# Performance work log

Measured on AMD Instinct MI355X. Metric: run time of the kernel, lower is better.

## Reference

```python
import jax, jax.numpy as jnp
import numpy as np

EMBED_DIM = 1024
NUM_HEADS = 16
HEAD_DIM = EMBED_DIM // NUM_HEADS


def setup_inputs() -> dict:
    key = jax.random.key(0)
    ks = jax.random.split(key, 7)
    B, S, E = 8, 1024, EMBED_DIM
    # xavier-uniform-like scale for in_proj_weight [3E, E]
    bound_in = float(np.sqrt(6.0 / (3 * E + E)))
    bound_out = float(np.sqrt(6.0 / (E + E)))
    return {
        "q": jax.random.normal(ks[0], (B, S, E), jnp.float32),
        "k": jax.random.normal(ks[1], (B, S, E), jnp.float32),
        "v": jax.random.normal(ks[2], (B, S, E), jnp.float32),
        "in_proj_weight": jax.random.uniform(ks[3], (3 * E, E), jnp.float32, -bound_in, bound_in),
        "in_proj_bias": jnp.zeros((3 * E,), jnp.float32),
        "out_proj_weight": jax.random.uniform(ks[4], (E, E), jnp.float32, -bound_out, bound_out),
        "out_proj_bias": jnp.zeros((E,), jnp.float32),
    }


def reference(q, k, v, in_proj_weight, in_proj_bias, out_proj_weight, out_proj_bias):
    B, S, E = q.shape
    H, D = NUM_HEADS, HEAD_DIM
    w_q, w_k, w_v = jnp.split(in_proj_weight, 3, axis=0)
    b_q, b_k, b_v = jnp.split(in_proj_bias, 3, axis=0)
    # packed in-projection: linear(x, W, b) = x @ W.T + b
    qp = q @ w_q.T + b_q
    kp = k @ w_k.T + b_k
    vp = v @ w_v.T + b_v
    # [B, S, E] -> [B, H, S, D]
    qh = qp.reshape(B, S, H, D).transpose(0, 2, 1, 3)
    kh = kp.reshape(B, S, H, D).transpose(0, 2, 1, 3)
    vh = vp.reshape(B, S, H, D).transpose(0, 2, 1, 3)
    scale = D ** -0.5
    # explicit full attention in fp32 (matches original fp32 cast path)
    scores = jnp.einsum("bhqd,bhkd->bhqk", qh, kh) * scale
    attn = jax.nn.softmax(scores, axis=-1)
    ctx = jnp.einsum("bhqk,bhkd->bhqd", attn, vh)  # [B, H, S, D]
    ctx = ctx.transpose(0, 2, 1, 3).reshape(B, S, E)
    out = ctx @ out_proj_weight.T + out_proj_bias
    return out
```

## Files before the change

### kernel.cpp

```cpp
#include <hip/hip_runtime.h>
#include <stdint.h>

#define TOK 8192
#define EDIM 1024
#define NH 16
#define HD 64
#define SEQ 1024
#define BATCH 8

typedef short bf16x8 __attribute__((ext_vector_type(8)));
typedef short bf16x4 __attribute__((ext_vector_type(4)));
typedef float f32x4 __attribute__((ext_vector_type(4)));
typedef float f32x16 __attribute__((ext_vector_type(16)));
typedef unsigned int u32x2 __attribute__((ext_vector_type(2)));
typedef unsigned int u32x4 __attribute__((ext_vector_type(4)));

__device__ __forceinline__ short f2bf(float f) {
  union { float f; uint32_t u; } c; c.f = f;
  uint32_t u = c.u;
  u += 0x7FFFu + ((u >> 16) & 1u);
  return (short)(u >> 16);
}
__device__ __forceinline__ float bf2f(short h) {
  union { uint32_t u; float f; } c; c.u = ((uint32_t)(uint16_t)h) << 16;
  return c.f;
}
__device__ __forceinline__ uint32_t bfr(float f) {
  union { float f; uint32_t u; } c; c.f = f;
  return (c.u + 0x8000u) >> 16;
}
__device__ __forceinline__ uint32_t cvtpk(float lo, float hi_) {
  uint32_t r;
  asm("v_cvt_pk_bf16_f32 %0, %1, %2" : "=v"(r) : "v"(lo), "v"(hi_));
  return r;
}

#define GLDS16(ldsp, gp) __builtin_amdgcn_global_load_lds( \
    (__attribute__((address_space(1))) void*)(gp),          \
    (__attribute__((address_space(3))) void*)(ldsp), 16, 0, 0)

__global__ __launch_bounds__(256) void cast_all(
    const float* __restrict__ q, const float* __restrict__ k,
    const float* __restrict__ v, const float* __restrict__ wi,
    const float* __restrict__ wo, short* __restrict__ dst) {
  const size_t NTOK = (size_t)TOK * EDIM;
  const size_t NWI = 3u * EDIM * EDIM;
  size_t i = ((size_t)blockIdx.x * 256 + threadIdx.x) * 4;
  const float* src;
  if (i < NTOK) src = q + i;
  else if (i < 2 * NTOK) src = k + (i - NTOK);
  else if (i < 3 * NTOK) src = v + (i - 2 * NTOK);
  else if (i < 3 * NTOK + NWI) src = wi + (i - 3 * NTOK);
  else src = wo + (i - 3 * NTOK - NWI);
  float4 f = *(const float4*)src;
  bf16x4 o;
  o[0] = f2bf(f.x); o[1] = f2bf(f.y); o[2] = f2bf(f.z); o[3] = f2bf(f.w);
  *(bf16x4*)(dst + i) = o;
}

#define GEMM_TILE9(KT, VMC, DOSTAGE)                                           \
  {                                                                            \
    asm volatile("s_waitcnt vmcnt(" VMC ")" ::: "memory");                     \
    __builtin_amdgcn_s_barrier();                                              \
    const short* Ab = lds + ((KT) & 3) * 12288;                                \
    const short* Bb = Ab + 8192;                                               \
    bf16x8 af[4], bv[4];                                                       \
    _Pragma("unroll")                                                          \
    for (int mi = 0; mi < 4; mi++)                                             \
      af[mi] = *(const bf16x8*)&Ab[(wrBase + mi * 16 + fr) * 32 + fg * 8];     \
    _Pragma("unroll")                                                          \
    for (int ni = 0; ni < 4; ni++)                                             \
      bv[ni] = *(const bf16x8*)&Bb[(wcBase + ni * 16 + fr) * 32 + fg * 8];     \
    if (DOSTAGE) {                                                             \
      char* d_ = (char*)lds + (((KT) + 3) & 3) * 24576 + t * 16;               \
      GLDS16(d_,         aS + ((KT) + 3) * 32);                                \
      GLDS16(d_ + 8192,  aS + ((KT) + 3) * 32 + 128 * 1024);                   \
      GLDS16(d_ + 16384, bS + ((KT) + 3) * 32);                                \
    }                                                                          \
    __builtin_amdgcn_s_setprio(1);                                             \
    _Pragma("unroll")                                                          \
    for (int mi = 0; mi < 4; mi++) {                                           \
      _Pragma("unroll")                                                        \
      for (int ni = 0; ni < 4; ni++)                                           \
        acc[mi][ni] = __builtin_amdgcn_mfma_f32_16x16x32_bf16(                 \
            af[mi], bv[ni], acc[mi][ni], 0, 0, 0);                             \
    }                                                                          \
    __builtin_amdgcn_s_setprio(0);                                             \
  }

template<int MODE>
__global__ __launch_bounds__(512, 1)
void gemm_bt9(const short* __restrict__ Abase, const short* __restrict__ Wbase,
              const float* __restrict__ biasBase, void* __restrict__ outv) {
  __shared__ short lds[49152];

  const int z = (MODE == 0) ? blockIdx.z : 0;
  const size_t NTOK = (size_t)TOK * EDIM;
  const short* A  = Abase + (size_t)z * NTOK;
  const short* Bw = Wbase + (size_t)z * EDIM * EDIM;
  const float* bias = biasBase + z * EDIM;

  const int t = threadIdx.x;
  const int l = t & 63, w = t >> 6;
  const int fr = l & 15, fg = l >> 4;
  const int wrBase = (w >> 1) * 64;
  const int wcBase = (w & 1) * 64;
  const int rowBase = blockIdx.x * 256;
  const int colBase = blockIdx.y * 128;

  f32x4 acc[4][4];
#pragma unroll
  for (int i = 0; i < 4; i++)
#pragma unroll
    for (int j = 0; j < 4; j++) acc[i][j] = (f32x4){0.f, 0.f, 0.f, 0.f};

  const short* aS = A  + (size_t)(rowBase + (t >> 2)) * EDIM + (t & 3) * 8;
  const short* bS = Bw + (size_t)(colBase + (t >> 2)) * EDIM + (t & 3) * 8;

#pragma unroll
  for (int s = 0; s < 3; s++) {
    char* d = (char*)lds + s * 24576 + t * 16;
    GLDS16(d,         aS + s * 32);
    GLDS16(d + 8192,  aS + s * 32 + 128 * 1024);
    GLDS16(d + 16384, bS + s * 32);
  }

#pragma unroll 1
  for (int kt = 0; kt < 30; kt++) {
    GEMM_TILE9(kt, "6", (kt <= 28));
  }
  GEMM_TILE9(30, "3", false);
  GEMM_TILE9(31, "0", false);

#pragma unroll
  for (int mi = 0; mi < 4; mi++)
#pragma unroll
    for (int ni = 0; ni < 4; ni++)
#pragma unroll
      for (int r = 0; r < 4; r++) {
        int grow = rowBase + wrBase + mi * 16 + fg * 4 + r;
        int gcol = colBase + wcBase + ni * 16 + fr;
        float v = acc[mi][ni][r] + bias[gcol];
        if (MODE == 0) {
          int b_ = grow >> 10, s_ = grow & 1023;
          int h_ = gcol >> 6,  d_ = gcol & 63;
          short* outp = (short*)outv + (size_t)z * NTOK;
          outp[((size_t)((b_ * NH + h_) * SEQ + s_) << 6) | d_] = f2bf(v);
        } else {
          ((float*)outv)[(size_t)grow * EDIM + gcol] = v;
        }
      }
}

__global__ __launch_bounds__(512)
void attn_fwd9(const short* __restrict__ proj, short* __restrict__ ctx) {
  __shared__ short lds[16384];

  const int t = threadIdx.x;
  const int l = t & 63, w = t >> 6;
  const int ln = l & 31, hi = l >> 5;

  const int n = blockIdx.x + 4 * (blockIdx.y + 16 * blockIdx.z);
  const int qt = (n >> 3) & 3;
  const int hl = (n & 7) | ((n >> 5) << 3);
  const int h = hl & 15, b = hl >> 4;

  const size_t NTOK = (size_t)TOK * EDIM;
  const size_t headOff = (size_t)(b * NH + h) * SEQ * HD;
  const short* Qp = proj + headOff;
  const short* Kp = proj + NTOK + headOff;
  const short* Vp = proj + 2 * NTOK + headOff;

  const int q0 = qt * 256;
  const int qrow = q0 + w * 32 + ln;

  const int kRow = t >> 3;
  const int kCol = ((t & 7) ^ (kRow & 7)) << 3;
  const int vd0  = w * 8;

  const float qscale = 0.18033688011112042f;
  bf16x8 bQ[4];
#pragma unroll
  for (int ds = 0; ds < 4; ds++) {
    bf16x8 v = *(const bf16x8*)(Qp + (size_t)qrow * HD + ds * 16 + hi * 8);
#pragma unroll
    for (int j = 0; j < 8; j++) v[j] = (short)bfr(bf2f(v[j]) * qscale);
    bQ[ds] = v;
  }

  float l_acc[4] = {0.f, 0.f, 0.f, 0.f};
  f32x16 ot[2];
#pragma unroll
  for (int i = 0; i < 16; i++) { ot[0][i] = 0.f; ot[1][i] = 0.f; }

  {
    GLDS16((char*)lds + t * 16, Kp + (size_t)kRow * HD + kCol);
    bf16x8 v0 = *(const bf16x8*)(Vp + (size_t)l * HD + vd0);
    char* VtB = (char*)lds + 8192;
#pragma unroll
    for (int jj = 0; jj < 8; jj++) {
      int d = vd0 + jj;
      *(short*)(VtB + d * 128 + (((l >> 3) ^ (d & 7)) << 4) + (l & 7) * 2) = v0[jj];
    }
  }
  __syncthreads();

  for (int jt = 0; jt < SEQ / 64; jt++) {
    const int bufByte = (jt & 1) << 14;
    const int nb = bufByte ^ (1 << 14);
    const bool have_next = (jt + 1 < SEQ / 64);

    bf16x8 nv0;
    if (have_next) {
      const int kv1 = (jt + 1) * 64;
      GLDS16((char*)lds + nb + t * 16, Kp + (size_t)(kv1 + kRow) * HD + kCol);
      nv0 = *(const bf16x8*)(Vp + (size_t)(kv1 + l) * HD + vd0);
    }

    f32x16 sa[2];
#pragma unroll
    for (int i = 0; i < 16; i++) { sa[0][i] = 0.f; sa[1][i] = 0.f; }
    __builtin_amdgcn_s_setprio(1);
#pragma unroll
    for (int ds = 0; ds < 4; ds++) {
#pragma unroll
      for (int kvb = 0; kvb < 2; kvb++) {
        int kv = kvb * 32 + ln;
        bf16x8 aK = *(const bf16x8*)((const char*)lds + bufByte + kv * 128 +
                                     (((ds * 2 + hi) ^ (kv & 7)) << 4));
        sa[kvb] = __builtin_amdgcn_mfma_f32_32x32x16_bf16(aK, bQ[ds], sa[kvb], 0, 0, 0);
      }
    }
    __builtin_amdgcn_s_setprio(0);

#pragma unroll
    for (int i = 0; i < 16; i++) {
      float p0 = exp2f(sa[0][i]);
      float p1 = exp2f(sa[1][i]);
      sa[0][i] = p0; sa[1][i] = p1;
      l_acc[i & 3] += p0 + p1;
    }

    bf16x8 pa[4];
#pragma unroll
    for (int ks = 0; ks < 4; ks++) {
      const int kvb = ks >> 1, hf = (ks & 1) * 8;
      uint32_t A1 = cvtpk(sa[kvb][hf + 0], sa[kvb][hf + 1]);
      uint32_t A2 = cvtpk(sa[kvb][hf + 2], sa[kvb][hf + 3]);
      uint32_t B1 = cvtpk(sa[kvb][hf + 4], sa[kvb][hf + 5]);
      uint32_t B2 = cvtpk(sa[kvb][hf + 6], sa[kvb][hf + 7]);
      u32x4 wds;
#if __has_builtin(__builtin_amdgcn_permlane32_swap)
      u32x2 r13 = __builtin_amdgcn_permlane32_swap(A1, B1, false, false);
      u32x2 r24 = __builtin_amdgcn_permlane32_swap(A2, B2, false, false);
      wds[0] = r13[0]; wds[2] = r13[1];
      wds[1] = r24[0]; wds[3] = r24[1];
#else
      uint32_t send1 = hi ? A1 : B1;
      uint32_t send2 = hi ? A2 : B2;
      uint32_t recv1 = (uint32_t)__shfl_xor((int)send1, 32);
      uint32_t recv2 = (uint32_t)__shfl_xor((int)send2, 32);
      wds[0] = hi ? recv1 : A1;
      wds[1] = hi ? recv2 : A2;
      wds[2] = hi ? B1 : recv1;
      wds[3] = hi ? B2 : recv2;
#endif
      pa[ks] = __builtin_bit_cast(bf16x8, wds);
    }

    const char* VtB = (const char*)lds + bufByte + 8192;
    __builtin_amdgcn_s_setprio(1);
#pragma unroll
    for (int ks = 0; ks < 4; ks++) {
#pragma unroll
      for (int dblk = 0; dblk < 2; dblk++) {
        int d = dblk * 32 + ln;
        bf16x8 aV = *(const bf16x8*)(VtB + d * 128 + (((ks * 2 + hi) ^ (d & 7)) << 4));
        ot[dblk] = __builtin_amdgcn_mfma_f32_32x32x16_bf16(aV, pa[ks], ot[dblk], 0, 0, 0);
      }
    }
    __builtin_amdgcn_s_setprio(0);

    if (have_next) {
      char* VtN = (char*)lds + nb + 8192;
#pragma unroll
      for (int jj = 0; jj < 8; jj++) {
        int d = vd0 + jj;
        *(short*)(VtN + d * 128 + (((l >> 3) ^ (d & 7)) << 4) + (l & 7) * 2) = nv0[jj];
      }
    }

    __syncthreads();
  }

  float l_run = (l_acc[0] + l_acc[1]) + (l_acc[2] + l_acc[3]);
  l_run += __shfl_xor(l_run, 32);
  float rl = 1.0f / l_run;

#pragma unroll
  for (int dblk = 0; dblk < 2; dblk++)
#pragma unroll
    for (int r = 0; r < 16; r++) {
      int d = dblk * 32 + (r & 3) + 8 * (r >> 2) + 4 * hi;
      int qrl = w * 32 + ln;
      int byteoff = qrl * 128 + (((d >> 3) ^ (qrl & 7)) << 4) + (d & 7) * 2;
      *(short*)((char*)lds + byteoff) = (short)bfr(ot[dblk][r] * rl);
    }
  __syncthreads();
#pragma unroll
  for (int i = 0; i < 4; i++) {
    int chunk = t * 4 + i;
    int row = chunk >> 3, c8 = chunk & 7;
    bf16x8 vv = *(const bf16x8*)((const char*)lds + row * 128 + ((c8 ^ (row & 7)) << 4));
    *(bf16x8*)(ctx + (size_t)(b * SEQ + q0 + row) * EDIM + h * HD + c8 * 8) = vv;
  }
}

extern "C" void kernel_launch(void* const* d_in, const int* in_sizes, int n_in,
                              void* d_out, int out_size, void* d_ws, size_t ws_size,
                              hipStream_t stream) {
  const float* q  = (const float*)d_in[0];
  const float* k  = (const float*)d_in[1];
  const float* v  = (const float*)d_in[2];
  const float* wi = (const float*)d_in[3];
  const float* bi = (const float*)d_in[4];
  const float* wo = (const float*)d_in[5];
  const float* bo = (const float*)d_in[6];
  float* out = (float*)d_out;

  short* ws = (short*)d_ws;
  const size_t NTOK = (size_t)TOK * EDIM;
  short* qkv_bf   = ws;
  short* w_in_bf  = qkv_bf + 3 * NTOK;
  short* w_out_bf = w_in_bf + 3 * (size_t)EDIM * EDIM;
  short* proj_bf  = w_out_bf + (size_t)EDIM * EDIM;
  short* ctx_bf   = qkv_bf;

  const size_t totalCast = 3 * NTOK + 3 * (size_t)EDIM * EDIM + (size_t)EDIM * EDIM;
  cast_all<<<dim3((unsigned)(totalCast / 4 / 256)), 256, 0, stream>>>(q, k, v, wi, wo, qkv_bf);

  gemm_bt9<0><<<dim3(TOK / 256, EDIM / 128, 3), 512, 0, stream>>>(qkv_bf, w_in_bf, bi, proj_bf);
  attn_fwd9<<<dim3(SEQ / 256, NH, BATCH), 512, 0, stream>>>(proj_bf, ctx_bf);
  gemm_bt9<1><<<dim3(TOK / 256, EDIM / 128, 1), 512, 0, stream>>>(ctx_bf, w_out_bf, bo, out);
}
```

Before: 171.6 us.

## Write V projection pre-transposed so attention loads V tiles via direct global-to-LDS

The in-projection GEMM epilogue now writes the V head output in [b,h,d,s] order rather than [b,h,s,d]. The attention kernel can then stage V tiles into LDS with the same swizzled global-to-LDS 16-byte loads used for K. This replaces per-element register loads and 8 scalar short LDS stores per thread per tile. The cost is moved into the GEMM epilogue, whose V stores become strided along s, which may hurt write coalescing there.

```diff
diff --git a/kernel.cpp b/kernel.cpp
--- a/kernel.cpp
+++ b/kernel.cpp
@@ -145,7 +145,10 @@
           int b_ = grow >> 10, s_ = grow & 1023;
           int h_ = gcol >> 6,  d_ = gcol & 63;
           short* outp = (short*)outv + (size_t)z * NTOK;
-          outp[((size_t)((b_ * NH + h_) * SEQ + s_) << 6) | d_] = f2bf(v);
+          size_t idx = (z == 2)
+              ? (((size_t)((b_ * NH + h_) * HD + d_) << 10) | s_)
+              : (((size_t)((b_ * NH + h_) * SEQ + s_) << 6) | d_);
+          outp[idx] = f2bf(v);
         } else {
           ((float*)outv)[(size_t)grow * EDIM + gcol] = v;
         }
@@ -153,7 +156,7 @@
 }
 
 __global__ __launch_bounds__(512)
-void attn_fwd9(const short* __restrict__ proj, short* __restrict__ ctx) {
+void attn_fwd10(const short* __restrict__ proj, short* __restrict__ ctx) {
   __shared__ short lds[16384];
 
   const int t = threadIdx.x;
@@ -167,16 +170,17 @@
 
   const size_t NTOK = (size_t)TOK * EDIM;
   const size_t headOff = (size_t)(b * NH + h) * SEQ * HD;
-  const short* Qp = proj + headOff;
-  const short* Kp = proj + NTOK + headOff;
-  const short* Vp = proj + 2 * NTOK + headOff;
+  const short* Qp  = proj + headOff;
+  const short* Kp  = proj + NTOK + headOff;
+  const short* VpT = proj + 2 * NTOK + headOff;
 
   const int q0 = qt * 256;
   const int qrow = q0 + w * 32 + ln;
 
-  const int kRow = t >> 3;
-  const int kCol = ((t & 7) ^ (kRow & 7)) << 3;
-  const int vd0  = w * 8;
+  const int sRow = t >> 3;
+  const int sColSw = ((t & 7) ^ (sRow & 7)) << 3;
+  const short* Ksrc0 = Kp  + (size_t)sRow * HD  + sColSw;
+  const short* Vsrc0 = VpT + (size_t)sRow * SEQ + sColSw;
 
   const float qscale = 0.18033688011112042f;
   bf16x8 bQ[4];
@@ -193,28 +197,17 @@
 #pragma unroll
   for (int i = 0; i < 16; i++) { ot[0][i] = 0.f; ot[1][i] = 0.f; }
 
-  {
-    GLDS16((char*)lds + t * 16, Kp + (size_t)kRow * HD + kCol);
-    bf16x8 v0 = *(const bf16x8*)(Vp + (size_t)l * HD + vd0);
-    char* VtB = (char*)lds + 8192;
-#pragma unroll
-    for (int jj = 0; jj < 8; jj++) {
-      int d = vd0 + jj;
-      *(short*)(VtB + d * 128 + (((l >> 3) ^ (d & 7)) << 4) + (l & 7) * 2) = v0[jj];
-    }
-  }
+  GLDS16((char*)lds + t * 16,        Ksrc0);
+  GLDS16((char*)lds + 8192 + t * 16, Vsrc0);
   __syncthreads();
 
   for (int jt = 0; jt < SEQ / 64; jt++) {
     const int bufByte = (jt & 1) << 14;
     const int nb = bufByte ^ (1 << 14);
-    const bool have_next = (jt + 1 < SEQ / 64);
-
-    bf16x8 nv0;
-    if (have_next) {
-      const int kv1 = (jt + 1) * 64;
-      GLDS16((char*)lds + nb + t * 16, Kp + (size_t)(kv1 + kRow) * HD + kCol);
-      nv0 = *(const bf16x8*)(Vp + (size_t)(kv1 + l) * HD + vd0);
+
+    if (jt + 1 < SEQ / 64) {
+      GLDS16((char*)lds + nb + t * 16,        Ksrc0 + (size_t)(jt + 1) * 64 * HD);
+      GLDS16((char*)lds + nb + 8192 + t * 16, Vsrc0 + (jt + 1) * 64);
     }
 
     f32x16 sa[2];
@@ -281,15 +274,6 @@
     }
     __builtin_amdgcn_s_setprio(0);
 
-    if (have_next) {
-      char* VtN = (char*)lds + nb + 8192;
-#pragma unroll
-      for (int jj = 0; jj < 8; jj++) {
-        int d = vd0 + jj;
-        *(short*)(VtN + d * 128 + (((l >> 3) ^ (d & 7)) << 4) + (l & 7) * 2) = nv0[jj];
-      }
-    }
-
     __syncthreads();
   }
 
@@ -340,6 +324,6 @@
   cast_all<<<dim3((unsigned)(totalCast / 4 / 256)), 256, 0, stream>>>(q, k, v, wi, wo, qkv_bf);
 
   gemm_bt9<0><<<dim3(TOK / 256, EDIM / 128, 3), 512, 0, stream>>>(qkv_bf, w_in_bf, bi, proj_bf);
-  attn_fwd9<<<dim3(SEQ / 256, NH, BATCH), 512, 0, stream>>>(proj_bf, ctx_bf);
+  attn_fwd10<<<dim3(SEQ / 256, NH, BATCH), 512, 0, stream>>>(proj_bf, ctx_bf);
   gemm_bt9<1><<<dim3(TOK / 256, EDIM / 128, 1), 512, 0, stream>>>(ctx_bf, w_out_bf, bo, out);
 }
```

New measurement: 172.3 us. Within noise of the previous version (+0.4%).
